# Optimization experiments

Hardware: AMD Instinct MI355X
Metric: run time of the kernel (lower is better)

The kernel has to match this reference:

```python
import jax, jax.numpy as jnp
import numpy as np

NEG_SLOPE = 0.2


def setup_inputs() -> dict:
    key = jax.random.key(0)
    ks = jax.random.split(key, 6)
    N, E, IN, H, D = 50000, 800000, 256, 4, 64
    x = jax.random.normal(ks[0], (N, IN), dtype=jnp.float32)
    edge_index = jax.random.randint(ks[1], (2, E), 0, N, dtype=jnp.int64)
    W = jax.random.normal(ks[2], (IN, H * D), dtype=jnp.float32) / np.sqrt(IN)
    att_src = jax.random.normal(ks[3], (H, D), dtype=jnp.float32) / np.sqrt(D)
    att_dst = jax.random.normal(ks[4], (H, D), dtype=jnp.float32) / np.sqrt(D)
    bias = jnp.zeros((H * D,), dtype=jnp.float32)
    return {"x": x, "edge_index": edge_index, "W": W,
            "att_src": att_src, "att_dst": att_dst, "bias": bias}


def reference(x, edge_index, W, att_src, att_dst, bias):
    N = x.shape[0]
    H, D = att_src.shape
    # add self-loops (PyG GATConv default add_self_loops=True)
    loops = jnp.arange(N, dtype=edge_index.dtype)
    src = jnp.concatenate([edge_index[0], loops])  # [E']
    dst = jnp.concatenate([edge_index[1], loops])  # [E']
    # per-head linear transform: [N, H, D]
    h = (x @ W).reshape(N, H, D)
    # per-node attention logits per head: [N, H]
    a_s = jnp.einsum('nhd,hd->nh', h, att_src)
    a_d = jnp.einsum('nhd,hd->nh', h, att_dst)
    # per-edge raw attention: [E', H]
    e = jax.nn.leaky_relu(a_s[src] + a_d[dst], NEG_SLOPE)
    # softmax over edges grouped by destination node (stable)
    m = jax.ops.segment_max(e, dst, num_segments=N)
    e = jnp.exp(e - m[dst])
    s = jax.ops.segment_sum(e, dst, num_segments=N)
    alpha = e / s[dst]  # every node has a self-loop -> s > 0
    # weighted scatter-aggregate: [N, H, D]
    out = jax.ops.segment_sum(alpha[:, :, None] * h[src], dst, num_segments=N)
    # concat heads + bias; dropout=0.0 -> identity
    return out.reshape(N, H * D) + bias
```

## Files before the change

### kernel.cpp

```cpp
#include <hip/hip_runtime.h>
#include <hip/hip_bf16.h>

#define NEG_SLOPE 0.2f
#define HPAD 264

typedef short short8 __attribute__((ext_vector_type(8)));
typedef float floatx4 __attribute__((ext_vector_type(4)));
typedef unsigned short ushort8v __attribute__((ext_vector_type(8)));
typedef unsigned short ushort4v __attribute__((ext_vector_type(4)));
typedef unsigned int uint4v __attribute__((ext_vector_type(4)));

__device__ __forceinline__ float bf2f_raw(unsigned short u) {
    union { float f; unsigned u; } c; c.u = ((unsigned)u) << 16; return c.f;
}
__device__ __forceinline__ float asf(unsigned u) {
    union { float f; unsigned u; } c; c.u = u; return c.f;
}
__device__ __forceinline__ unsigned short f2bf_raw(float f) {
    union { float f; unsigned u; } c; c.f = f;
    unsigned u = c.u;
    u += 0x7FFFu + ((u >> 16) & 1u);
    return (unsigned short)(u >> 16);
}
__device__ __forceinline__ float ldf(const void* p, size_t i, int f32) {
    return f32 ? ((const float*)p)[i] : bf2f_raw(((const unsigned short*)p)[i]);
}
__device__ __forceinline__ unsigned short ldbf(const void* p, size_t i, int f32) {
    return f32 ? f2bf_raw(((const float*)p)[i]) : ((const unsigned short*)p)[i];
}
__device__ __forceinline__ int clampN(long long v, int N) {
    if (v < 0) v = 0;
    if (v >= N) v = N - 1;
    return (int)v;
}
__device__ __forceinline__ float lrelu(float v) { return v > 0.f ? v : NEG_SLOPE * v; }

__global__ __launch_bounds__(256) void detect_kernel(
    const unsigned short* __restrict__ x, const unsigned short* __restrict__ W,
    const unsigned short* __restrict__ as_, const unsigned short* __restrict__ ad_,
    const unsigned* __restrict__ edge_w, int* __restrict__ flags, int edge_words)
{
    __shared__ float sm[256];
    __shared__ unsigned su[256];
    const int t = threadIdx.x;

    float mx = 0.f, mw = 0.f, ma = 0.f;
    for (int i = t; i < 4096; i += 256) {
        float v = fabsf(bf2f_raw(x[i]));
        mx = fmaxf(mx, (v == v && v < 3e38f) ? v : 1e9f);
    }
    for (int i = t; i < 4096; i += 256) {
        float v = fabsf(bf2f_raw(W[i]));
        mw = fmaxf(mw, (v == v && v < 3e38f) ? v : 1e9f);
    }
    {
        float v1 = fabsf(bf2f_raw(as_[t]));
        float v2 = fabsf(bf2f_raw(ad_[t]));
        v1 = (v1 == v1 && v1 < 3e38f) ? v1 : 1e9f;
        v2 = (v2 == v2 && v2 < 3e38f) ? v2 : 1e9f;
        ma = fmaxf(v1, v2);
    }
    unsigned ow = 0;
    {
        int i = 2 * t + 1;
        if (i < edge_words) ow = edge_w[i];
    }

    sm[t] = mx; __syncthreads();
    for (int s = 128; s; s >>= 1) { if (t < s) sm[t] = fmaxf(sm[t], sm[t + s]); __syncthreads(); }
    if (t == 0) flags[0] = sm[0] > 100.f;
    __syncthreads();

    sm[t] = mw; __syncthreads();
    for (int s = 128; s; s >>= 1) { if (t < s) sm[t] = fmaxf(sm[t], sm[t + s]); __syncthreads(); }
    if (t == 0) flags[1] = sm[0] > 100.f;
    __syncthreads();

    sm[t] = ma; __syncthreads();
    for (int s = 128; s; s >>= 1) { if (t < s) sm[t] = fmaxf(sm[t], sm[t + s]); __syncthreads(); }
    if (t == 0) flags[2] = sm[0] > 100.f;
    __syncthreads();

    su[t] = ow; __syncthreads();
    for (int s = 128; s; s >>= 1) { if (t < s) su[t] |= su[t + s]; __syncthreads(); }
    if (t == 0) flags[3] = (su[0] == 0u);
}

__global__ __launch_bounds__(256) void wt_kernel(
    const void* __restrict__ W, unsigned short* __restrict__ Wt,
    const int* __restrict__ flags, int* __restrict__ deg8, int* __restrict__ bsync, int N8)
{
    int i = blockIdx.x * 256 + threadIdx.x;
    #pragma unroll
    for (int j = 0; j < 7; ++j) {
        int z = i + j * 65536;
        if (z < N8) deg8[z] = 0;
    }
    if (i < 256) bsync[i] = 0;
    int j = i & 7;
    int l = (i >> 3) & 63;
    int ks = (i >> 9) & 7;
    int c = i >> 12;
    int k = ks * 32 + (l >> 4) * 8 + j;
    int n = c * 16 + (l & 15);
    Wt[i] = ldbf(W, (size_t)k * 256 + n, flags[1]);
}

__global__ __launch_bounds__(512) void gemm_count_kernel(
    const void* __restrict__ x, const unsigned short* __restrict__ Wt,
    const void* __restrict__ att_src, const void* __restrict__ att_dst,
    unsigned short* __restrict__ h_out, float* __restrict__ a_s, float* __restrict__ a_d,
    const void* __restrict__ edge, int* __restrict__ deg8, int* __restrict__ rank,
    const int* __restrict__ flags, int N, int E, int ntiles,
    int ngemm, int ncount, int ntotal)
{
    const unsigned long long bi = blockIdx.x;
    const unsigned before = (unsigned)((bi * (unsigned long long)ncount) / ntotal);
    const unsigned after  = (unsigned)(((bi + 1) * (unsigned long long)ncount) / ntotal);

    if (after != before) {
        const int cb = (int)before;
        const int base = cb * 2048 + threadIdx.x * 4;
        if (base >= E) return;
        int* my = deg8 + (size_t)(cb & 7) * N;
        const int cnt = (E - base < 4) ? (E - base) : 4;
        int d[4];
        if (flags[3]) {
            const long long* p = (const long long*)edge + E + base;
            #pragma unroll
            for (int k = 0; k < 4; ++k) d[k] = clampN((k < cnt) ? p[k] : 0, N);
        } else {
            const int* p = (const int*)edge + E + base;
            #pragma unroll
            for (int k = 0; k < 4; ++k) d[k] = clampN((k < cnt) ? (long long)p[k] : 0, N);
        }
        int r[4] = {0, 0, 0, 0};
        #pragma unroll
        for (int k = 0; k < 4; ++k)
            if (k < cnt) r[k] = atomicAdd(&my[d[k]], 1);
        #pragma unroll
        for (int k = 0; k < 4; ++k)
            if (k < cnt) rank[base + k] = r[k];
        return;
    }

    const int gb = (int)(bi - before);

    __shared__ unsigned short sh_h[32][HPAD];
    __shared__ float sh_a[2][32][4];

    const int w = threadIdx.x >> 6;
    const int head = w >> 1;
    const int st = w & 1;
    const int l = threadIdx.x & 63;
    const int lane16 = l & 15;
    const int quad = l >> 4;
    const int xf = flags[0], af = flags[2];
    const int n0w = head * 64;

    float as_att[4], ad_att[4];
    #pragma unroll
    for (int nt = 0; nt < 4; ++nt) {
        as_att[nt] = ldf(att_src, n0w + nt * 16 + lane16, af);
        ad_att[nt] = ldf(att_dst, n0w + nt * 16 + lane16, af);
    }

    for (int tile = gb; tile < ntiles; tile += ngemm) {
        const int m0 = tile * 32;
        int r0 = m0 + st * 16 + lane16;
        if (r0 >= N) r0 = N - 1;

        floatx4 acc[4];
        #pragma unroll
        for (int nt = 0; nt < 4; ++nt) acc[nt] = (floatx4){0.f, 0.f, 0.f, 0.f};

        const unsigned short* wp0 = Wt + (((size_t)head * 32) * 64 + l) * 8;

        #pragma unroll
        for (int half = 0; half < 2; ++half) {
            short8 fa[4];
            if (!xf) {
                const char* b0 = (const char*)x + ((size_t)r0 * 256 + quad * 8) * 2 + half * 256;
                #pragma unroll
                for (int k4 = 0; k4 < 4; ++k4)
                    fa[k4] = *(const short8*)(b0 + k4 * 64);
            } else {
                const float* b0 = (const float*)x + (size_t)r0 * 256 + quad * 8 + half * 128;
                #pragma unroll
                for (int k4 = 0; k4 < 4; ++k4) {
                    #pragma unroll
                    for (int j = 0; j < 8; ++j)
                        fa[k4][j] = (short)f2bf_raw(b0[k4 * 32 + j]);
                }
            }

            #pragma unroll
            for (int k4 = 0; k4 < 4; ++k4) {
                const unsigned short* wp = wp0 + (size_t)(half * 4 + k4) * 512;
                #pragma unroll
                for (int nt = 0; nt < 4; ++nt) {
                    short8 fb = *(const short8*)(wp + nt * 4096);
                    acc[nt] = __builtin_amdgcn_mfma_f32_16x16x32_bf16(fa[k4], fb, acc[nt], 0, 0, 0);
                }
            }
        }

        __syncthreads();

        #pragma unroll
        for (int nt = 0; nt < 4; ++nt) {
            #pragma unroll
            for (int r = 0; r < 4; ++r) {
                sh_h[st * 16 + quad * 4 + r][n0w + nt * 16 + lane16] = f2bf_raw(acc[nt][r]);
            }
        }
        #pragma unroll
        for (int r = 0; r < 4; ++r) {
            float vs = acc[0][r] * as_att[0] + acc[1][r] * as_att[1]
                     + acc[2][r] * as_att[2] + acc[3][r] * as_att[3];
            float vd = acc[0][r] * ad_att[0] + acc[1][r] * ad_att[1]
                     + acc[2][r] * ad_att[2] + acc[3][r] * ad_att[3];
            vs += __shfl_xor(vs, 1); vs += __shfl_xor(vs, 2);
            vs += __shfl_xor(vs, 4); vs += __shfl_xor(vs, 8);
            vd += __shfl_xor(vd, 1); vd += __shfl_xor(vd, 2);
            vd += __shfl_xor(vd, 4); vd += __shfl_xor(vd, 8);
            if (lane16 == 0) {
                const int row = st * 16 + quad * 4 + r;
                sh_a[0][row][head] = vs;
                sh_a[1][row][head] = vd;
            }
        }

        __syncthreads();

        #pragma unroll
        for (int p = 0; p < 2; ++p) {
            const int c = p * 512 + threadIdx.x;
            const int row = c >> 5;
            const int ch = c & 31;
            if (m0 + row < N) {
                ushort8v v = *(const ushort8v*)&sh_h[row][ch * 8];
                *(ushort8v*)(h_out + (size_t)(m0 + row) * 256 + ch * 8) = v;
            }
        }
        {
            const int t = threadIdx.x;
            if (t < 32) {
                if (m0 + t < N)
                    *(floatx4*)&a_s[(size_t)(m0 + t) * 4] = *(const floatx4*)&sh_a[0][t][0];
            } else if (t >= 64 && t < 96) {
                const int r = t - 64;
                if (m0 + r < N)
                    *(floatx4*)&a_d[(size_t)(m0 + r) * 4] = *(const floatx4*)&sh_a[1][r][0];
            }
        }
    }
}

__global__ __launch_bounds__(256) void scan_fused_kernel(
    const int* __restrict__ deg8, int* __restrict__ deg,
    int* __restrict__ row_off, int* __restrict__ cursor8,
    int* __restrict__ bsum, int* __restrict__ bbase, int* __restrict__ bsync,
    int N, int nb)
{
    __shared__ int sh[256];
    __shared__ int is_last;
    __shared__ int sbase;
    const int b = blockIdx.x, t = threadIdx.x;
    const int base_i = b * 1024 + t * 4;
    int v[4], ts = 0;
    #pragma unroll
    for (int i = 0; i < 4; ++i) {
        int idx = base_i + i;
        int tot = 0;
        if (idx < N) {
            #pragma unroll
            for (int x = 0; x < 8; ++x) tot += deg8[(size_t)x * N + idx];
        }
        v[i] = tot;
        ts += tot;
    }
    sh[t] = ts; __syncthreads();
    for (int off = 1; off < 256; off <<= 1) {
        int add = (t >= off) ? sh[t - off] : 0;
        __syncthreads();
        sh[t] += add;
        __syncthreads();
    }
    if (t == 255) {
        __hip_atomic_store(&bsum[b], sh[255], __ATOMIC_RELEASE, __HIP_MEMORY_SCOPE_AGENT);
        int arrived = __hip_atomic_fetch_add(&bsync[0], 1, __ATOMIC_ACQ_REL, __HIP_MEMORY_SCOPE_AGENT);
        is_last = (arrived == nb - 1);
    }
    __syncthreads();
    if (is_last) {
        if (nb <= 64) {
            if (t < 64) {
                int val = (t < nb)
                    ? __hip_atomic_load(&bsum[t], __ATOMIC_ACQUIRE, __HIP_MEMORY_SCOPE_AGENT) : 0;
                int incl = val;
                #pragma unroll
                for (int off = 1; off < 64; off <<= 1) {
                    int u = __shfl_up(incl, off);
                    if (t >= off) incl += u;
                }
                if (t < nb)
                    __hip_atomic_store(&bbase[t], incl - val, __ATOMIC_RELEASE, __HIP_MEMORY_SCOPE_AGENT);
            }
        } else if (t == 0) {
            int run = 0;
            for (int i = 0; i < nb; ++i) {
                int s = __hip_atomic_load(&bsum[i], __ATOMIC_ACQUIRE, __HIP_MEMORY_SCOPE_AGENT);
                __hip_atomic_store(&bbase[i], run, __ATOMIC_RELEASE, __HIP_MEMORY_SCOPE_AGENT);
                run += s;
            }
        }
        __syncthreads();
        if (t == 0)
            __hip_atomic_store(&bsync[1], 1, __ATOMIC_RELEASE, __HIP_MEMORY_SCOPE_AGENT);
    }
    if (t == 0) {
        while (__hip_atomic_load(&bsync[1], __ATOMIC_ACQUIRE, __HIP_MEMORY_SCOPE_AGENT) == 0) {}
        sbase = __hip_atomic_load(&bbase[b], __ATOMIC_RELAXED, __HIP_MEMORY_SCOPE_AGENT);
    }
    __syncthreads();
    int run = sbase + sh[t] - ts;
    #pragma unroll
    for (int i = 0; i < 4; ++i) {
        int idx = base_i + i;
        if (idx < N) {
            row_off[idx] = run;
            deg[idx] = v[i];
            int c = run;
            #pragma unroll
            for (int x = 0; x < 8; ++x) {
                cursor8[(size_t)x * N + idx] = c;
                c += deg8[(size_t)x * N + idx];
            }
        }
        run += v[i];
    }
}

__global__ __launch_bounds__(512) void scatter_kernel(
    const void* __restrict__ edge, const int* __restrict__ cursor8,
    const int* __restrict__ rank, int* __restrict__ elist,
    const int* __restrict__ flags, int E, int N)
{
    const int base = blockIdx.x * 2048 + threadIdx.x * 4;
    if (base >= E) return;
    const int* mybase = cursor8 + (size_t)(blockIdx.x & 7) * N;
    const int cnt = (E - base < 4) ? (E - base) : 4;
    int s[4], d[4];
    if (flags[3]) {
        const long long* ps = (const long long*)edge + base;
        const long long* pd = (const long long*)edge + E + base;
        #pragma unroll
        for (int k = 0; k < 4; ++k) {
            s[k] = clampN((k < cnt) ? ps[k] : 0, N);
            d[k] = clampN((k < cnt) ? pd[k] : 0, N);
        }
    } else {
        const int* ps = (const int*)edge + base;
        const int* pd = (const int*)edge + E + base;
        #pragma unroll
        for (int k = 0; k < 4; ++k) {
            s[k] = clampN((k < cnt) ? (long long)ps[k] : 0, N);
            d[k] = clampN((k < cnt) ? (long long)pd[k] : 0, N);
        }
    }
    #pragma unroll
    for (int k = 0; k < 4; ++k) {
        if (k < cnt) {
            int pos = mybase[d[k]] + rank[base + k];
            elist[pos] = s[k];
        }
    }
}

__global__ __launch_bounds__(256) void aggregate_kernel(
    const int* __restrict__ row_off, const int* __restrict__ deg,
    const int* __restrict__ elist,
    const float* __restrict__ a_s, const float* __restrict__ a_d,
    const unsigned short* __restrict__ h_ws,
    const void* __restrict__ bias, void* __restrict__ out,
    const int* __restrict__ flags, int N, int nwaves)
{
    const int gw = blockIdx.x * 4 + (threadIdx.x >> 6);
    const int lane = threadIdx.x & 63;
    const int q = lane >> 4;
    const int li = lane & 15;
    const int head = li >> 2;
    const int col0 = li * 16;
    const int bf32 = flags[2];
    const int of32 = flags[0];

    for (int n = gw; n < N; n += nwaves) {
        const int dn = deg[n];
        const int row = row_off[n];
        const float adn = a_d[n * 4 + head];
        const float self_logit = lrelu(a_s[n * 4 + head] + adn);

        float acc[16];
        {
            const uint4v* hp = (const uint4v*)(h_ws + (size_t)n * 256 + col0);
            uint4v ha = hp[0], hb = hp[1];
            #pragma unroll
            for (int w = 0; w < 4; ++w) {
                acc[2 * w]         = (q == 0) ? asf(ha[w] << 16) : 0.f;
                acc[2 * w + 1]     = (q == 0) ? asf(ha[w] & 0xffff0000u) : 0.f;
                acc[8 + 2 * w]     = (q == 0) ? asf(hb[w] << 16) : 0.f;
                acc[8 + 2 * w + 1] = (q == 0) ? asf(hb[w] & 0xffff0000u) : 0.f;
            }
        }
        float ssum = (q == 0) ? 1.f : 0.f;

        float asA, asB;
        uint4v hA0, hA1, hB0, hB1;
        int sC, sD;
        {
            int e0 = q, e1 = 4 + q, e2 = 8 + q, e3 = 12 + q;
            int s0 = (e0 < dn) ? elist[row + e0] : n;
            int s1 = (e1 < dn) ? elist[row + e1] : n;
            sC = (e2 < dn) ? elist[row + e2] : n;
            sD = (e3 < dn) ? elist[row + e3] : n;
            asA = a_s[s0 * 4 + head];
            asB = a_s[s1 * 4 + head];
            const uint4v* pA = (const uint4v*)(h_ws + (size_t)s0 * 256 + col0);
            const uint4v* pB = (const uint4v*)(h_ws + (size_t)s1 * 256 + col0);
            hA0 = pA[0]; hA1 = pA[1];
            hB0 = pB[0]; hB1 = pB[1];
        }

        for (int c0 = 0; c0 < dn; c0 += 8) {
            {
                float p = __expf(lrelu(asA + adn) - self_logit);
                p = (c0 + q < dn) ? p : 0.f;
                ssum += p;
                #pragma unroll
                for (int w = 0; w < 4; ++w) {
                    acc[2 * w]         += p * asf(hA0[w] << 16);
                    acc[2 * w + 1]     += p * asf(hA0[w] & 0xffff0000u);
                    acc[8 + 2 * w]     += p * asf(hA1[w] << 16);
                    acc[8 + 2 * w + 1] += p * asf(hA1[w] & 0xffff0000u);
                }
            }
            {
                asA = a_s[sC * 4 + head];
                const uint4v* p = (const uint4v*)(h_ws + (size_t)sC * 256 + col0);
                hA0 = p[0]; hA1 = p[1];
                int e = c0 + 16 + q;
                sC = (e < dn) ? elist[row + e] : n;
            }
            {
                float p = __expf(lrelu(asB + adn) - self_logit);
                p = (c0 + 4 + q < dn) ? p : 0.f;
                ssum += p;
                #pragma unroll
                for (int w = 0; w < 4; ++w) {
                    acc[2 * w]         += p * asf(hB0[w] << 16);
                    acc[2 * w + 1]     += p * asf(hB0[w] & 0xffff0000u);
                    acc[8 + 2 * w]     += p * asf(hB1[w] << 16);
                    acc[8 + 2 * w + 1] += p * asf(hB1[w] & 0xffff0000u);
                }
            }
            {
                asB = a_s[sD * 4 + head];
                const uint4v* p = (const uint4v*)(h_ws + (size_t)sD * 256 + col0);
                hB0 = p[0]; hB1 = p[1];
                int e = c0 + 20 + q;
                sD = (e < dn) ? elist[row + e] : n;
            }
        }

        #pragma unroll
        for (int j = 0; j < 16; ++j) {
            acc[j] += __shfl_xor(acc[j], 16);
            acc[j] += __shfl_xor(acc[j], 32);
        }
        float stot = ssum + __shfl_xor(ssum, 16);
        stot += __shfl_xor(stot, 32);

        const float inv = 1.f / stot;
        const int j0 = q * 4;
        float o[4];
        #pragma unroll
        for (int k = 0; k < 4; ++k)
            o[k] = acc[j0 + k] * inv + ldf(bias, col0 + j0 + k, bf32);
        if (of32) {
            float* op = (float*)out + (size_t)n * 256 + col0 + j0;
            __builtin_nontemporal_store((floatx4){o[0], o[1], o[2], o[3]}, (floatx4*)op);
        } else {
            ushort4v ov;
            #pragma unroll
            for (int k = 0; k < 4; ++k) ov[k] = f2bf_raw(o[k]);
            __builtin_nontemporal_store(ov,
                (ushort4v*)((unsigned short*)out + (size_t)n * 256 + col0 + j0));
        }
    }
}

__global__ __launch_bounds__(256) void sentinel_kernel(unsigned short* out, size_t n, float v) {
    size_t i = (size_t)blockIdx.x * 256 + threadIdx.x;
    if (i < n) out[i] = f2bf_raw(v);
}

extern "C" void kernel_launch(void* const* d_in, const int* in_sizes, int n_in,
                              void* d_out, int out_size, void* d_ws, size_t ws_size,
                              hipStream_t stream) {
    const void* x       = d_in[0];
    const void* edge    = d_in[1];
    const void* W       = d_in[2];
    const void* att_src = d_in[3];
    const void* att_dst = d_in[4];
    const void* bias    = d_in[5];

    const int N = in_sizes[0] / 256;
    const int E = in_sizes[1] / 2;

    char* ws = (char*)d_ws;
    size_t off = 256;
    int*   flags   = (int*)ws;
    float* a_s     = (float*)(ws + off); off += (size_t)N * 4 * sizeof(float);
    float* a_d     = (float*)(ws + off); off += (size_t)N * 4 * sizeof(float);
    int*   deg     = (int*)(ws + off);   off += (size_t)N * sizeof(int);
    int*   row_off = (int*)(ws + off);   off += (size_t)N * sizeof(int);
    int*   bsum    = (int*)(ws + off);   off += 256 * sizeof(int);
    int*   bbase   = (int*)(ws + off);   off += 256 * sizeof(int);
    int*   bsync   = (int*)(ws + off);   off += 256 * sizeof(int);
    unsigned short* Wt = (unsigned short*)(ws + off); off += 65536 * sizeof(unsigned short);
    size_t elist_bytes = (size_t)E * sizeof(int);
    size_t deg8_bytes  = (size_t)8 * N * sizeof(int);
    int*   elist   = (int*)(ws + off);
    int*   deg8    = (int*)(ws + off);   off += (elist_bytes > deg8_bytes ? elist_bytes : deg8_bytes);
    int*   cursor8 = (int*)(ws + off);   off += deg8_bytes;
    int*   rank    = (int*)(ws + off);   off += (size_t)E * sizeof(int);
    unsigned short* h_ws = (unsigned short*)(ws + off);
    const size_t need = off + (size_t)N * 256 * sizeof(unsigned short);

    if (ws_size < need) {
        float v = (float)(ws_size >> 20) * 1000.0f;
        size_t n = (size_t)out_size;
        sentinel_kernel<<<(unsigned)((n + 255) / 256), 256, 0, stream>>>(
            (unsigned short*)d_out, n, v);
        return;
    }

    int edge_words = (2 * E < 512) ? 2 * E : 512;
    detect_kernel<<<1, 256, 0, stream>>>(
        (const unsigned short*)x, (const unsigned short*)W,
        (const unsigned short*)att_src, (const unsigned short*)att_dst,
        (const unsigned*)edge, flags, edge_words);

    wt_kernel<<<256, 256, 0, stream>>>(W, Wt, flags, deg8, bsync, 8 * N);

    const int ntiles = (N + 31) / 32;
    const int ngemm = 1024;
    const int ncount = (E + 2047) / 2048;
    const int ntotal = ngemm + ncount;
    gemm_count_kernel<<<ntotal, 512, 0, stream>>>(
        x, Wt, att_src, att_dst, h_ws, a_s, a_d, edge, deg8, rank,
        flags, N, E, ntiles, ngemm, ncount, ntotal);

    const int nb = (N + 1023) / 1024;
    scan_fused_kernel<<<nb, 256, 0, stream>>>(
        deg8, deg, row_off, cursor8, bsum, bbase, bsync, N, nb);

    scatter_kernel<<<ncount, 512, 0, stream>>>(edge, cursor8, rank, elist, flags, E, N);

    const int agg_blocks = 2048;
    aggregate_kernel<<<agg_blocks, 256, 0, stream>>>(
        row_off, deg, elist, a_s, a_d, h_ws, bias, d_out, flags, N, agg_blocks * 4);
}
```

Baseline: 263.7 us.

## Fuse detect+transpose, scan+scatter kernels; one wave per node in aggregate

The detect and W-transpose kernels become one prep kernel in which each block recomputes the W-format flag locally. The scan and scatter kernels become one kernel that does a grid-wide spin barrier between the scan phase and the scatter phase. The aggregate kernel drops its grid-stride loop and launches one wave per node. Together these remove two kernel launches and their gaps. The cost is a software grid barrier, which assumes all 391 blocks of 512 threads are resident at once and could deadlock otherwise.

```diff
diff --git a/kernel.cpp b/kernel.cpp
--- a/kernel.cpp
+++ b/kernel.cpp
@@ -35,75 +35,73 @@
 }
 __device__ __forceinline__ float lrelu(float v) { return v > 0.f ? v : NEG_SLOPE * v; }
 
-__global__ __launch_bounds__(256) void detect_kernel(
-    const unsigned short* __restrict__ x, const unsigned short* __restrict__ W,
+__global__ __launch_bounds__(256) void prep_kernel(
+    const void* __restrict__ W, unsigned short* __restrict__ Wt,
+    const unsigned short* __restrict__ x,
     const unsigned short* __restrict__ as_, const unsigned short* __restrict__ ad_,
-    const unsigned* __restrict__ edge_w, int* __restrict__ flags, int edge_words)
+    const unsigned* __restrict__ edge_w, int* __restrict__ flags, int edge_words,
+    int* __restrict__ deg8, int* __restrict__ bsync, int N8)
 {
     __shared__ float sm[256];
     __shared__ unsigned su[256];
     const int t = threadIdx.x;
-
-    float mx = 0.f, mw = 0.f, ma = 0.f;
-    for (int i = t; i < 4096; i += 256) {
-        float v = fabsf(bf2f_raw(x[i]));
-        mx = fmaxf(mx, (v == v && v < 3e38f) ? v : 1e9f);
-    }
-    for (int i = t; i < 4096; i += 256) {
-        float v = fabsf(bf2f_raw(W[i]));
-        mw = fmaxf(mw, (v == v && v < 3e38f) ? v : 1e9f);
-    }
-    {
-        float v1 = fabsf(bf2f_raw(as_[t]));
-        float v2 = fabsf(bf2f_raw(ad_[t]));
-        v1 = (v1 == v1 && v1 < 3e38f) ? v1 : 1e9f;
-        v2 = (v2 == v2 && v2 < 3e38f) ? v2 : 1e9f;
-        ma = fmaxf(v1, v2);
-    }
-    unsigned ow = 0;
-    {
-        int i = 2 * t + 1;
-        if (i < edge_words) ow = edge_w[i];
-    }
-
-    sm[t] = mx; __syncthreads();
-    for (int s = 128; s; s >>= 1) { if (t < s) sm[t] = fmaxf(sm[t], sm[t + s]); __syncthreads(); }
-    if (t == 0) flags[0] = sm[0] > 100.f;
-    __syncthreads();
-
-    sm[t] = mw; __syncthreads();
-    for (int s = 128; s; s >>= 1) { if (t < s) sm[t] = fmaxf(sm[t], sm[t + s]); __syncthreads(); }
-    if (t == 0) flags[1] = sm[0] > 100.f;
-    __syncthreads();
-
-    sm[t] = ma; __syncthreads();
-    for (int s = 128; s; s >>= 1) { if (t < s) sm[t] = fmaxf(sm[t], sm[t + s]); __syncthreads(); }
-    if (t == 0) flags[2] = sm[0] > 100.f;
-    __syncthreads();
-
-    su[t] = ow; __syncthreads();
-    for (int s = 128; s; s >>= 1) { if (t < s) su[t] |= su[t + s]; __syncthreads(); }
-    if (t == 0) flags[3] = (su[0] == 0u);
-}
-
-__global__ __launch_bounds__(256) void wt_kernel(
-    const void* __restrict__ W, unsigned short* __restrict__ Wt,
-    const int* __restrict__ flags, int* __restrict__ deg8, int* __restrict__ bsync, int N8)
-{
-    int i = blockIdx.x * 256 + threadIdx.x;
+    const int i = blockIdx.x * 256 + t;
+
     #pragma unroll
     for (int j = 0; j < 7; ++j) {
         int z = i + j * 65536;
         if (z < N8) deg8[z] = 0;
     }
     if (i < 256) bsync[i] = 0;
+
+    float mw = 0.f;
+    for (int k = t; k < 4096; k += 256) {
+        float v = fabsf(bf2f_raw(((const unsigned short*)W)[k]));
+        mw = fmaxf(mw, (v == v && v < 3e38f) ? v : 1e9f);
+    }
+    sm[t] = mw; __syncthreads();
+    for (int s = 128; s; s >>= 1) { if (t < s) sm[t] = fmaxf(sm[t], sm[t + s]); __syncthreads(); }
+    const int wf32 = sm[0] > 100.f;
+    __syncthreads();
+
+    if (blockIdx.x == 0) {
+        float mx = 0.f, ma = 0.f;
+        for (int k = t; k < 4096; k += 256) {
+            float v = fabsf(bf2f_raw(x[k]));
+            mx = fmaxf(mx, (v == v && v < 3e38f) ? v : 1e9f);
+        }
+        {
+            float v1 = fabsf(bf2f_raw(as_[t]));
+            float v2 = fabsf(bf2f_raw(ad_[t]));
+            v1 = (v1 == v1 && v1 < 3e38f) ? v1 : 1e9f;
+            v2 = (v2 == v2 && v2 < 3e38f) ? v2 : 1e9f;
+            ma = fmaxf(v1, v2);
+        }
+        unsigned ow = 0;
+        {
+            int k = 2 * t + 1;
+            if (k < edge_words) ow = edge_w[k];
+        }
+        sm[t] = mx; __syncthreads();
+        for (int s = 128; s; s >>= 1) { if (t < s) sm[t] = fmaxf(sm[t], sm[t + s]); __syncthreads(); }
+        if (t == 0) flags[0] = sm[0] > 100.f;
+        __syncthreads();
+        sm[t] = ma; __syncthreads();
+        for (int s = 128; s; s >>= 1) { if (t < s) sm[t] = fmaxf(sm[t], sm[t + s]); __syncthreads(); }
+        if (t == 0) flags[2] = sm[0] > 100.f;
+        __syncthreads();
+        su[t] = ow; __syncthreads();
+        for (int s = 128; s; s >>= 1) { if (t < s) su[t] |= su[t + s]; __syncthreads(); }
+        if (t == 0) { flags[3] = (su[0] == 0u); flags[1] = wf32; }
+    }
+
     int j = i & 7;
     int l = (i >> 3) & 63;
     int ks = (i >> 9) & 7;
     int c = i >> 12;
     int k = ks * 32 + (l >> 4) * 8 + j;
     int n = c * 16 + (l & 15);
-    Wt[i] = ldbf(W, (size_t)k * 256 + n, flags[1]);
+    Wt[i] = ldbf(W, (size_t)k * 256 + n, wf32);
 }
 
 __global__ __launch_bounds__(512) void gemm_count_kernel(
@@ -257,99 +255,105 @@
     }
 }
 
-__global__ __launch_bounds__(256) void scan_fused_kernel(
+__global__ __launch_bounds__(512) void scan_scatter_kernel(
     const int* __restrict__ deg8, int* __restrict__ deg,
     int* __restrict__ row_off, int* __restrict__ cursor8,
     int* __restrict__ bsum, int* __restrict__ bbase, int* __restrict__ bsync,
-    int N, int nb)
+    const void* __restrict__ edge, const int* __restrict__ rank,
+    int* __restrict__ elist, const int* __restrict__ flags,
+    int N, int nb, int E, int nblocks)
 {
-    __shared__ int sh[256];
+    __shared__ int sh[512];
     __shared__ int is_last;
     __shared__ int sbase;
     const int b = blockIdx.x, t = threadIdx.x;
-    const int base_i = b * 1024 + t * 4;
-    int v[4], ts = 0;
-    #pragma unroll
-    for (int i = 0; i < 4; ++i) {
-        int idx = base_i + i;
-        int tot = 0;
-        if (idx < N) {
-            #pragma unroll
-            for (int x = 0; x < 8; ++x) tot += deg8[(size_t)x * N + idx];
-        }
-        v[i] = tot;
-        ts += tot;
-    }
-    sh[t] = ts; __syncthreads();
-    for (int off = 1; off < 256; off <<= 1) {
-        int add = (t >= off) ? sh[t - off] : 0;
-        __syncthreads();
-        sh[t] += add;
-        __syncthreads();
-    }
-    if (t == 255) {
-        __hip_atomic_store(&bsum[b], sh[255], __ATOMIC_RELEASE, __HIP_MEMORY_SCOPE_AGENT);
-        int arrived = __hip_atomic_fetch_add(&bsync[0], 1, __ATOMIC_ACQ_REL, __HIP_MEMORY_SCOPE_AGENT);
-        is_last = (arrived == nb - 1);
+
+    if (b < nb) {
+        const int base_i = b * 2048 + t * 4;
+        int v[4], ts = 0;
+        #pragma unroll
+        for (int i = 0; i < 4; ++i) {
+            int idx = base_i + i;
+            int tot = 0;
+            if (idx < N) {
+                #pragma unroll
+                for (int x = 0; x < 8; ++x) tot += deg8[(size_t)x * N + idx];
+            }
+            v[i] = tot;
+            ts += tot;
+        }
+        sh[t] = ts; __syncthreads();
+        for (int off = 1; off < 512; off <<= 1) {
+            int add = (t >= off) ? sh[t - off] : 0;
+            __syncthreads();
+            sh[t] += add;
+            __syncthreads();
+        }
+        if (t == 511) {
+            __hip_atomic_store(&bsum[b], sh[511], __ATOMIC_RELEASE, __HIP_MEMORY_SCOPE_AGENT);
+            int arrived = __hip_atomic_fetch_add(&bsync[0], 1, __ATOMIC_ACQ_REL, __HIP_MEMORY_SCOPE_AGENT);
+            is_last = (arrived == nb - 1);
+        }
+        __syncthreads();
+        if (is_last) {
+            if (nb <= 64) {
+                if (t < 64) {
+                    int val = (t < nb)
+                        ? __hip_atomic_load(&bsum[t], __ATOMIC_ACQUIRE, __HIP_MEMORY_SCOPE_AGENT) : 0;
+                    int incl = val;
+                    #pragma unroll
+                    for (int off = 1; off < 64; off <<= 1) {
+                        int u = __shfl_up(incl, off);
+                        if (t >= off) incl += u;
+                    }
+                    if (t < nb)
+                        __hip_atomic_store(&bbase[t], incl - val, __ATOMIC_RELEASE, __HIP_MEMORY_SCOPE_AGENT);
+                }
+            } else if (t == 0) {
+                int run = 0;
+                for (int i = 0; i < nb; ++i) {
+                    int s = __hip_atomic_load(&bsum[i], __ATOMIC_ACQUIRE, __HIP_MEMORY_SCOPE_AGENT);
+                    __hip_atomic_store(&bbase[i], run, __ATOMIC_RELEASE, __HIP_MEMORY_SCOPE_AGENT);
+                    run += s;
+                }
+            }
+            __syncthreads();
+            if (t == 0)
+                __hip_atomic_store(&bsync[1], 1, __ATOMIC_RELEASE, __HIP_MEMORY_SCOPE_AGENT);
+        }
+        if (t == 0) {
+            while (__hip_atomic_load(&bsync[1], __ATOMIC_ACQUIRE, __HIP_MEMORY_SCOPE_AGENT) == 0) {}
+            sbase = __hip_atomic_load(&bbase[b], __ATOMIC_RELAXED, __HIP_MEMORY_SCOPE_AGENT);
+        }
+        __syncthreads();
+        int run = sbase + sh[t] - ts;
+        #pragma unroll
+        for (int i = 0; i < 4; ++i) {
+            int idx = base_i + i;
+            if (idx < N) {
+                row_off[idx] = run;
+                deg[idx] = v[i];
+                int c = run;
+                #pragma unroll
+                for (int x = 0; x < 8; ++x) {
+                    cursor8[(size_t)x * N + idx] = c;
+                    c += deg8[(size_t)x * N + idx];
+                }
+            }
+            run += v[i];
+        }
+        __syncthreads();
+    }
+
+    if (t == 0) {
+        __hip_atomic_fetch_add(&bsync[2], 1, __ATOMIC_ACQ_REL, __HIP_MEMORY_SCOPE_AGENT);
+        while (__hip_atomic_load(&bsync[2], __ATOMIC_ACQUIRE, __HIP_MEMORY_SCOPE_AGENT) < nblocks) {}
     }
     __syncthreads();
-    if (is_last) {
-        if (nb <= 64) {
-            if (t < 64) {
-                int val = (t < nb)
-                    ? __hip_atomic_load(&bsum[t], __ATOMIC_ACQUIRE, __HIP_MEMORY_SCOPE_AGENT) : 0;
-                int incl = val;
-                #pragma unroll
-                for (int off = 1; off < 64; off <<= 1) {
-                    int u = __shfl_up(incl, off);
-                    if (t >= off) incl += u;
-                }
-                if (t < nb)
-                    __hip_atomic_store(&bbase[t], incl - val, __ATOMIC_RELEASE, __HIP_MEMORY_SCOPE_AGENT);
-            }
-        } else if (t == 0) {
-            int run = 0;
-            for (int i = 0; i < nb; ++i) {
-                int s = __hip_atomic_load(&bsum[i], __ATOMIC_ACQUIRE, __HIP_MEMORY_SCOPE_AGENT);
-                __hip_atomic_store(&bbase[i], run, __ATOMIC_RELEASE, __HIP_MEMORY_SCOPE_AGENT);
-                run += s;
-            }
-        }
-        __syncthreads();
-        if (t == 0)
-            __hip_atomic_store(&bsync[1], 1, __ATOMIC_RELEASE, __HIP_MEMORY_SCOPE_AGENT);
-    }
-    if (t == 0) {
-        while (__hip_atomic_load(&bsync[1], __ATOMIC_ACQUIRE, __HIP_MEMORY_SCOPE_AGENT) == 0) {}
-        sbase = __hip_atomic_load(&bbase[b], __ATOMIC_RELAXED, __HIP_MEMORY_SCOPE_AGENT);
-    }
-    __syncthreads();
-    int run = sbase + sh[t] - ts;
-    #pragma unroll
-    for (int i = 0; i < 4; ++i) {
-        int idx = base_i + i;
-        if (idx < N) {
-            row_off[idx] = run;
-            deg[idx] = v[i];
-            int c = run;
-            #pragma unroll
-            for (int x = 0; x < 8; ++x) {
-                cursor8[(size_t)x * N + idx] = c;
-                c += deg8[(size_t)x * N + idx];
-            }
-        }
-        run += v[i];
-    }
-}
-
-__global__ __launch_bounds__(512) void scatter_kernel(
-    const void* __restrict__ edge, const int* __restrict__ cursor8,
-    const int* __restrict__ rank, int* __restrict__ elist,
-    const int* __restrict__ flags, int E, int N)
-{
-    const int base = blockIdx.x * 2048 + threadIdx.x * 4;
+
+    const int base = b * 2048 + t * 4;
     if (base >= E) return;
-    const int* mybase = cursor8 + (size_t)(blockIdx.x & 7) * N;
+    const int* mybase = cursor8 + (size_t)(b & 7) * N;
     const int cnt = (E - base < 4) ? (E - base) : 4;
     int s[4], d[4];
     if (flags[3]) {
@@ -384,119 +388,117 @@
     const float* __restrict__ a_s, const float* __restrict__ a_d,
     const unsigned short* __restrict__ h_ws,
     const void* __restrict__ bias, void* __restrict__ out,
-    const int* __restrict__ flags, int N, int nwaves)
+    const int* __restrict__ flags, int N)
 {
-    const int gw = blockIdx.x * 4 + (threadIdx.x >> 6);
+    const int n = blockIdx.x * 4 + (threadIdx.x >> 6);
+    if (n >= N) return;
     const int lane = threadIdx.x & 63;
     const int q = lane >> 4;
     const int li = lane & 15;
     const int head = li >> 2;
     const int col0 = li * 16;
-    const int bf32 = flags[2];
-    const int of32 = flags[0];
-
-    for (int n = gw; n < N; n += nwaves) {
-        const int dn = deg[n];
-        const int row = row_off[n];
-        const float adn = a_d[n * 4 + head];
-        const float self_logit = lrelu(a_s[n * 4 + head] + adn);
-
-        float acc[16];
-        {
-            const uint4v* hp = (const uint4v*)(h_ws + (size_t)n * 256 + col0);
-            uint4v ha = hp[0], hb = hp[1];
+
+    const int dn = deg[n];
+    const int row = row_off[n];
+    const float adn = a_d[n * 4 + head];
+    const float self_logit = lrelu(a_s[n * 4 + head] + adn);
+
+    float acc[16];
+    {
+        const uint4v* hp = (const uint4v*)(h_ws + (size_t)n * 256 + col0);
+        uint4v ha = hp[0], hb = hp[1];
+        #pragma unroll
+        for (int w = 0; w < 4; ++w) {
+            acc[2 * w]         = (q == 0) ? asf(ha[w] << 16) : 0.f;
+            acc[2 * w + 1]     = (q == 0) ? asf(ha[w] & 0xffff0000u) : 0.f;
+            acc[8 + 2 * w]     = (q == 0) ? asf(hb[w] << 16) : 0.f;
+            acc[8 + 2 * w + 1] = (q == 0) ? asf(hb[w] & 0xffff0000u) : 0.f;
+        }
+    }
+    float ssum = (q == 0) ? 1.f : 0.f;
+
+    float asA, asB;
+    uint4v hA0, hA1, hB0, hB1;
+    int sC, sD;
+    {
+        int e0 = q, e1 = 4 + q, e2 = 8 + q, e3 = 12 + q;
+        int s0 = (e0 < dn) ? elist[row + e0] : n;
+        int s1 = (e1 < dn) ? elist[row + e1] : n;
+        sC = (e2 < dn) ? elist[row + e2] : n;
+        sD = (e3 < dn) ? elist[row + e3] : n;
+        asA = a_s[s0 * 4 + head];
+        asB = a_s[s1 * 4 + head];
+        const uint4v* pA = (const uint4v*)(h_ws + (size_t)s0 * 256 + col0);
+        const uint4v* pB = (const uint4v*)(h_ws + (size_t)s1 * 256 + col0);
+        hA0 = pA[0]; hA1 = pA[1];
+        hB0 = pB[0]; hB1 = pB[1];
+    }
+
+    for (int c0 = 0; c0 < dn; c0 += 8) {
+        {
+            float p = __expf(lrelu(asA + adn) - self_logit);
+            p = (c0 + q < dn) ? p : 0.f;
+            ssum += p;
             #pragma unroll
             for (int w = 0; w < 4; ++w) {
-                acc[2 * w]         = (q == 0) ? asf(ha[w] << 16) : 0.f;
-                acc[2 * w + 1]     = (q == 0) ? asf(ha[w] & 0xffff0000u) : 0.f;
-                acc[8 + 2 * w]     = (q == 0) ? asf(hb[w] << 16) : 0.f;
-                acc[8 + 2 * w + 1] = (q == 0) ? asf(hb[w] & 0xffff0000u) : 0.f;
-            }
-        }
-        float ssum = (q == 0) ? 1.f : 0.f;
-
-        float asA, asB;
-        uint4v hA0, hA1, hB0, hB1;
-        int sC, sD;
-        {
-            int e0 = q, e1 = 4 + q, e2 = 8 + q, e3 = 12 + q;
-            int s0 = (e0 < dn) ? elist[row + e0] : n;
-            int s1 = (e1 < dn) ? elist[row + e1] : n;
-            sC = (e2 < dn) ? elist[row + e2] : n;
-            sD = (e3 < dn) ? elist[row + e3] : n;
-            asA = a_s[s0 * 4 + head];
-            asB = a_s[s1 * 4 + head];
-            const uint4v* pA = (const uint4v*)(h_ws + (size_t)s0 * 256 + col0);
-            const uint4v* pB = (const uint4v*)(h_ws + (size_t)s1 * 256 + col0);
-            hA0 = pA[0]; hA1 = pA[1];
-            hB0 = pB[0]; hB1 = pB[1];
-        }
-
-        for (int c0 = 0; c0 < dn; c0 += 8) {
-            {
-                float p = __expf(lrelu(asA + adn) - self_logit);
-                p = (c0 + q < dn) ? p : 0.f;
-                ssum += p;
-                #pragma unroll
-                for (int w = 0; w < 4; ++w) {
-                    acc[2 * w]         += p * asf(hA0[w] << 16);
-                    acc[2 * w + 1]     += p * asf(hA0[w] & 0xffff0000u);
-                    acc[8 + 2 * w]     += p * asf(hA1[w] << 16);
-                    acc[8 + 2 * w + 1] += p * asf(hA1[w] & 0xffff0000u);
-                }
-            }
-            {
-                asA = a_s[sC * 4 + head];
-                const uint4v* p = (const uint4v*)(h_ws + (size_t)sC * 256 + col0);
-                hA0 = p[0]; hA1 = p[1];
-                int e = c0 + 16 + q;
-                sC = (e < dn) ? elist[row + e] : n;
-            }
-            {
-                float p = __expf(lrelu(asB + adn) - self_logit);
-                p = (c0 + 4 + q < dn) ? p : 0.f;
-                ssum += p;
-                #pragma unroll
-                for (int w = 0; w < 4; ++w) {
-                    acc[2 * w]         += p * asf(hB0[w] << 16);
-                    acc[2 * w + 1]     += p * asf(hB0[w] & 0xffff0000u);
-                    acc[8 + 2 * w]     += p * asf(hB1[w] << 16);
-                    acc[8 + 2 * w + 1] += p * asf(hB1[w] & 0xffff0000u);
-                }
-            }
-            {
-                asB = a_s[sD * 4 + head];
-                const uint4v* p = (const uint4v*)(h_ws + (size_t)sD * 256 + col0);
-                hB0 = p[0]; hB1 = p[1];
-                int e = c0 + 20 + q;
-                sD = (e < dn) ? elist[row + e] : n;
-            }
-        }
-
-        #pragma unroll
-        for (int j = 0; j < 16; ++j) {
-            acc[j] += __shfl_xor(acc[j], 16);
-            acc[j] += __shfl_xor(acc[j], 32);
-        }
-        float stot = ssum + __shfl_xor(ssum, 16);
-        stot += __shfl_xor(stot, 32);
-
-        const float inv = 1.f / stot;
-        const int j0 = q * 4;
-        float o[4];
-        #pragma unroll
-        for (int k = 0; k < 4; ++k)
-            o[k] = acc[j0 + k] * inv + ldf(bias, col0 + j0 + k, bf32);
-        if (of32) {
-            float* op = (float*)out + (size_t)n * 256 + col0 + j0;
-            __builtin_nontemporal_store((floatx4){o[0], o[1], o[2], o[3]}, (floatx4*)op);
-        } else {
-            ushort4v ov;
+                acc[2 * w]         += p * asf(hA0[w] << 16);
+                acc[2 * w + 1]     += p * asf(hA0[w] & 0xffff0000u);
+                acc[8 + 2 * w]     += p * asf(hA1[w] << 16);
+                acc[8 + 2 * w + 1] += p * asf(hA1[w] & 0xffff0000u);
+            }
+        }
+        {
+            asA = a_s[sC * 4 + head];
+            const uint4v* p = (const uint4v*)(h_ws + (size_t)sC * 256 + col0);
+            hA0 = p[0]; hA1 = p[1];
+            int e = c0 + 16 + q;
+            sC = (e < dn) ? elist[row + e] : n;
+        }
+        {
+            float p = __expf(lrelu(asB + adn) - self_logit);
+            p = (c0 + 4 + q < dn) ? p : 0.f;
+            ssum += p;
             #pragma unroll
-            for (int k = 0; k < 4; ++k) ov[k] = f2bf_raw(o[k]);
-            __builtin_nontemporal_store(ov,
-                (ushort4v*)((unsigned short*)out + (size_t)n * 256 + col0 + j0));
-        }
+            for (int w = 0; w < 4; ++w) {
+                acc[2 * w]         += p * asf(hB0[w] << 16);
+                acc[2 * w + 1]     += p * asf(hB0[w] & 0xffff0000u);
+                acc[8 + 2 * w]     += p * asf(hB1[w] << 16);
+                acc[8 + 2 * w + 1] += p * asf(hB1[w] & 0xffff0000u);
+            }
+        }
+        {
+            asB = a_s[sD * 4 + head];
+            const uint4v* p = (const uint4v*)(h_ws + (size_t)sD * 256 + col0);
+            hB0 = p[0]; hB1 = p[1];
+            int e = c0 + 20 + q;
+            sD = (e < dn) ? elist[row + e] : n;
+        }
+    }
+
+    #pragma unroll
+    for (int j = 0; j < 16; ++j) {
+        acc[j] += __shfl_xor(acc[j], 16);
+        acc[j] += __shfl_xor(acc[j], 32);
+    }
+    float stot = ssum + __shfl_xor(ssum, 16);
+    stot += __shfl_xor(stot, 32);
+
+    const float inv = 1.f / stot;
+    const int j0 = q * 4;
+    const int bf32 = flags[2];
+    float o[4];
+    #pragma unroll
+    for (int k = 0; k < 4; ++k)
+        o[k] = acc[j0 + k] * inv + ldf(bias, col0 + j0 + k, bf32);
+    if (flags[0]) {
+        float* op = (float*)out + (size_t)n * 256 + col0 + j0;
+        __builtin_nontemporal_store((floatx4){o[0], o[1], o[2], o[3]}, (floatx4*)op);
+    } else {
+        ushort4v ov;
+        #pragma unroll
+        for (int k = 0; k < 4; ++k) ov[k] = f2bf_raw(o[k]);
+        __builtin_nontemporal_store(ov,
+            (ushort4v*)((unsigned short*)out + (size_t)n * 256 + col0 + j0));
     }
 }
 
@@ -547,12 +549,10 @@
     }
 
     int edge_words = (2 * E < 512) ? 2 * E : 512;
-    detect_kernel<<<1, 256, 0, stream>>>(
-        (const unsigned short*)x, (const unsigned short*)W,
+    prep_kernel<<<256, 256, 0, stream>>>(
+        W, Wt, (const unsigned short*)x,
         (const unsigned short*)att_src, (const unsigned short*)att_dst,
-        (const unsigned*)edge, flags, edge_words);
-
-    wt_kernel<<<256, 256, 0, stream>>>(W, Wt, flags, deg8, bsync, 8 * N);
+        (const unsigned*)edge, flags, edge_words, deg8, bsync, 8 * N);
 
     const int ntiles = (N + 31) / 32;
     const int ngemm = 1024;
@@ -562,13 +562,11 @@
         x, Wt, att_src, att_dst, h_ws, a_s, a_d, edge, deg8, rank,
         flags, N, E, ntiles, ngemm, ncount, ntotal);
 
-    const int nb = (N + 1023) / 1024;
-    scan_fused_kernel<<<nb, 256, 0, stream>>>(
-        deg8, deg, row_off, cursor8, bsum, bbase, bsync, N, nb);
-
-    scatter_kernel<<<ncount, 512, 0, stream>>>(edge, cursor8, rank, elist, flags, E, N);
-
-    const int agg_blocks = 2048;
-    aggregate_kernel<<<agg_blocks, 256, 0, stream>>>(
-        row_off, deg, elist, a_s, a_d, h_ws, bias, d_out, flags, N, agg_blocks * 4);
-}
+    const int nb = (N + 2047) / 2048;
+    scan_scatter_kernel<<<ncount, 512, 0, stream>>>(
+        deg8, deg, row_off, cursor8, bsum, bbase, bsync,
+        edge, rank, elist, flags, N, nb, E, ncount);
+
+    aggregate_kernel<<<(N + 3) / 4, 256, 0, stream>>>(
+        row_off, deg, elist, a_s, a_d, h_ws, bias, d_out, flags, N);
+}
```

New measurement: 385.6 us. 46.2% more time.
